# Optimization experiments

Hardware: AMD Instinct MI355X
Metric: run time of the kernel (lower is better)

Reference implementation:

```python
import jax, jax.numpy as jnp
import numpy as np

Z, N, K, W = 131072, 64, 64, 32


def setup_inputs() -> dict:
    key = jax.random.key(0)
    k1, k2, k3 = jax.random.split(key, 3)
    features = jax.random.normal(k1, (Z, N), dtype=jnp.float32)
    # dense realization of the CG-derived mixing tensor 'wkij'
    mixing_matrix = jax.random.normal(k2, (W, K, N, N), dtype=jnp.float32) * 0.05
    weight = jax.random.normal(k3, (W,), dtype=jnp.float32)
    return {"features": features, "mixing_matrix": mixing_matrix, "weight": weight}


def reference(features, mixing_matrix, weight):
    # torch: einsum('w,wkij,zi,zj->zk', weight, mixing_matrix, features, features)
    # Contract the small path axis w first -> [K, N, N] (cheap, tiny output),
    # then the bilinear square over z. einsum chooses a GEMM-style path; the
    # [Z, N, N] outer-product side is the memory-bound part.
    M = jnp.einsum('w,wkij->kij', weight, mixing_matrix)  # [K, N, N]
    out = jnp.einsum('kij,zi,zj->zk', M, features, features)  # [Z, K]
    return out
```

## Files before the change

### kernel.cpp

```cpp
#include <hip/hip_runtime.h>
#include <stdint.h>

typedef __attribute__((ext_vector_type(8))) short short8;
typedef __attribute__((ext_vector_type(4))) float f32x4;
typedef __attribute__((ext_vector_type(2))) float v2f;

#define NCHUNK 32
#define BROWS  136
#define XROWD  130

__device__ __forceinline__ unsigned short f2bf_rne(float f) {
  unsigned u = __builtin_bit_cast(unsigned, f);
  u += 0x7fffu + ((u >> 16) & 1u);
  return (unsigned short)(u >> 16);
}
__device__ __forceinline__ unsigned pack_bf2(float p0, float p1) {
  return __builtin_amdgcn_perm(__builtin_bit_cast(unsigned, p1),
                               __builtin_bit_cast(unsigned, p0), 0x07060302u);
}

__global__ __launch_bounds__(256) void prep_kernel(const float* __restrict__ mix,
                                                   const float* __restrict__ wgt,
                                                   unsigned short* __restrict__ Bp) {
  __shared__ float4 red[256];
  const int tid = threadIdx.x;
  const int ws  = tid >> 6;
  const int tt  = tid & 63;
  const int t4  = blockIdx.x * 64 + tt;
  const float4* m4 = (const float4*)mix;
  float ax = 0.f, ay = 0.f, az = 0.f, aw = 0.f;
#pragma unroll
  for (int wi = 0; wi < 8; ++wi) {
    const int w = ws * 8 + wi;
    const float s = wgt[w];
    const float4 v = m4[w * 65536 + t4];
    ax += s * v.x; ay += s * v.y; az += s * v.z; aw += s * v.w;
  }
  red[tid] = (float4){ax, ay, az, aw};
  __syncthreads();
  if (tid < 64) {
    const float4 a = red[tid], b = red[tid + 64], c = red[tid + 128], d = red[tid + 192];
    ushort4 r;
    r.x = f2bf_rne(a.x + b.x + c.x + d.x);
    r.y = f2bf_rne(a.y + b.y + c.y + d.y);
    r.z = f2bf_rne(a.z + b.z + c.z + d.z);
    r.w = f2bf_rne(a.w + b.w + c.w + d.w);
    ((ushort4*)Bp)[blockIdx.x * 64 + tid] = r;
  }
}

__global__ __launch_bounds__(256, 2) void gemm_kernel(const float* __restrict__ X,
                                                      const unsigned short* __restrict__ Bp,
                                                      float* __restrict__ out) {
  __shared__ unsigned short ldsB[2][64 * BROWS];
  __shared__ unsigned ldsX[64 * XROWD];

  const int tid  = threadIdx.x;
  const int lane = tid & 63;
  const int wv   = tid >> 6;
  const int m    = lane & 15;
  const int q    = lane >> 4;
  const int zblk = blockIdx.x * 256;

  {
    const float4* X4 = (const float4*)(X + (size_t)zblk * 64);
    const int rr = lane;
    const int ms = rr & 15;
    const int fd = (rr >> 4) & 1;
    const int ih = rr >> 5;
    const int zl = wv * 64 + fd * 32 + ms;
    const int zh = zl + 16;
    const int dcol = wv * 32 + ms * 2 + fd;
#pragma unroll
    for (int c4 = 0; c4 < 8; ++c4) {
      const float4 ve = X4[zl * 16 + ih * 8 + c4];
      const float4 vo = X4[zh * 16 + ih * 8 + c4];
      float ae[4], ao[4];
      *(float4*)ae = ve; *(float4*)ao = vo;
      const int i0 = ih * 32 + c4 * 4;
#pragma unroll
      for (int r = 0; r < 4; ++r) {
        const unsigned pk = (unsigned)f2bf_rne(ae[r]) | ((unsigned)f2bf_rne(ao[r]) << 16);
        ldsX[(i0 + r) * XROWD + dcol] = pk;
      }
    }
  }
  {
#pragma unroll
    for (int it = 0; it < 4; ++it) {
      const int lin = tid + it * 256;
      const int row = lin >> 4;
      const int cc  = lin & 15;
      const uint4 v = *(const uint4*)(Bp + row * 4096 + cc * 8);
      *(uint4*)(&ldsB[0][row * BROWS + cc * 8]) = v;
    }
  }

  v2f jv2[4][8];
  {
    const float4* X4g = (const float4*)X;
#pragma unroll
    for (int f = 0; f < 4; ++f) {
      const int zg = zblk + wv * 64 + f * 16 + m;
#pragma unroll
      for (int h = 0; h < 2; ++h) {
        const float4 a = X4g[zg * 16 + h * 8 + q * 2];
        const float4 b = X4g[zg * 16 + h * 8 + q * 2 + 1];
        jv2[f][h * 4 + 0] = v2f{a.x, a.y};
        jv2[f][h * 4 + 1] = v2f{a.z, a.w};
        jv2[f][h * 4 + 2] = v2f{b.x, b.y};
        jv2[f][h * 4 + 3] = v2f{b.z, b.w};
      }
    }
  }

  f32x4 acc[4][4];
#pragma unroll
  for (int f = 0; f < 4; ++f)
#pragma unroll
    for (int g = 0; g < 4; ++g) acc[f][g] = f32x4{0.f, 0.f, 0.f, 0.f};

  __syncthreads();

  for (int c = 0; c < NCHUNK; ++c) {
    uint4 pre[4];
    const int cn = (c + 1) & (NCHUNK - 1);
#pragma unroll
    for (int it = 0; it < 4; ++it) {
      const int lin = tid + it * 256;
      const int row = lin >> 4;
      const int cc  = lin & 15;
      pre[it] = *(const uint4*)(Bp + row * 4096 + cn * 128 + cc * 8);
    }

    const unsigned short* Bl = ldsB[c & 1];

#pragma unroll
    for (int il = 0; il < 2; ++il) {
      const int i = c * 2 + il;
      const uint2 sv = *(const uint2*)(ldsX + i * XROWD + wv * 32 + m * 2);
      float sf[4];
      sf[0] = __builtin_bit_cast(float, sv.x << 16);
      sf[1] = __builtin_bit_cast(float, sv.x & 0xffff0000u);
      sf[2] = __builtin_bit_cast(float, sv.y << 16);
      sf[3] = __builtin_bit_cast(float, sv.y & 0xffff0000u);
#pragma unroll
      for (int h = 0; h < 2; ++h) {
        const unsigned short* bb = Bl + m * BROWS + il * 64 + h * 32 + q * 8;
        const short8 b0 = *(const short8*)(bb);
        const short8 b1 = *(const short8*)(bb + 16 * BROWS);
        const short8 b2 = *(const short8*)(bb + 32 * BROWS);
        const short8 b3 = *(const short8*)(bb + 48 * BROWS);
#pragma unroll
        for (int f = 0; f < 4; ++f) {
          const v2f s2 = v2f{sf[f], sf[f]};
          union { unsigned u[4]; short8 v; } A;
#pragma unroll
          for (int e = 0; e < 4; ++e) {
            const v2f pr = s2 * jv2[f][h * 4 + e];
            A.u[e] = pack_bf2(pr[0], pr[1]);
          }
          acc[f][0] = __builtin_amdgcn_mfma_f32_16x16x32_bf16(A.v, b0, acc[f][0], 0, 0, 0);
          acc[f][1] = __builtin_amdgcn_mfma_f32_16x16x32_bf16(A.v, b1, acc[f][1], 0, 0, 0);
          acc[f][2] = __builtin_amdgcn_mfma_f32_16x16x32_bf16(A.v, b2, acc[f][2], 0, 0, 0);
          acc[f][3] = __builtin_amdgcn_mfma_f32_16x16x32_bf16(A.v, b3, acc[f][3], 0, 0, 0);
        }
      }
    }

    {
      unsigned short* dst = ldsB[(c + 1) & 1];
#pragma unroll
      for (int it = 0; it < 4; ++it) {
        const int lin = tid + it * 256;
        const int row = lin >> 4;
        const int cc  = lin & 15;
        *(uint4*)(&dst[row * BROWS + cc * 8]) = pre[it];
      }
    }
    __syncthreads();
  }

#pragma unroll
  for (int f = 0; f < 4; ++f) {
    const int zr = zblk + wv * 64 + f * 16 + q * 4;
#pragma unroll
    for (int g = 0; g < 4; ++g)
#pragma unroll
      for (int r = 0; r < 4; ++r)
        out[(size_t)(zr + r) * 64 + g * 16 + m] = acc[f][g][r];
  }
}

extern "C" void kernel_launch(void* const* d_in, const int* in_sizes, int n_in,
                              void* d_out, int out_size, void* d_ws, size_t ws_size,
                              hipStream_t stream) {
  const float* X   = (const float*)d_in[0];
  const float* mix = (const float*)d_in[1];
  const float* wgt = (const float*)d_in[2];
  float* out = (float*)d_out;
  unsigned short* Bp = (unsigned short*)d_ws;

  prep_kernel<<<1024, 256, 0, stream>>>(mix, wgt, Bp);
  gemm_kernel<<<512, 256, 0, stream>>>(X, Bp, out);
}
```

Baseline: 163.9 us.

## Fold M into upper-triangular form and skip half the bilinear MFMA work

Adds a kernel that symmetrizes each M_k by adding the transpose into the upper triangle and zeroing the lower triangle. The GEMM can then skip the j<i half-blocks for the second half of the i chunks, cutting MFMA and A-operand construction work. The GEMM block also shrinks to 128 rows with higher occupancy (launch bounds 4, 1024 blocks). It streams the per-chunk scale features through a small double-buffered LDS array instead of staging a full transposed X tile. The trade-offs are an extra kernel launch, a second bf16 rounding of the summed M entries, and the B operand still being streamed for the skipped blocks.

Result: slower. 249.4 us (+52.2%).

```diff
diff --git a/kernel.cpp b/kernel.cpp
--- a/kernel.cpp
+++ b/kernel.cpp
@@ -7,12 +7,14 @@
 
 #define NCHUNK 32
 #define BROWS  136
-#define XROWD  130
 
 __device__ __forceinline__ unsigned short f2bf_rne(float f) {
   unsigned u = __builtin_bit_cast(unsigned, f);
   u += 0x7fffu + ((u >> 16) & 1u);
   return (unsigned short)(u >> 16);
+}
+__device__ __forceinline__ float bf2f(unsigned short s) {
+  return __builtin_bit_cast(float, ((unsigned)s) << 16);
 }
 __device__ __forceinline__ unsigned pack_bf2(float p0, float p1) {
   return __builtin_amdgcn_perm(__builtin_bit_cast(unsigned, p1),
@@ -49,59 +51,54 @@
   }
 }
 
-__global__ __launch_bounds__(256, 2) void gemm_kernel(const float* __restrict__ X,
+__global__ __launch_bounds__(256) void symm_kernel(unsigned short* __restrict__ Bp) {
+  unsigned short* B = Bp + (size_t)blockIdx.x * 4096;
+  for (int t = threadIdx.x; t < 4096; t += 256) {
+    const int i = t >> 6, j = t & 63;
+    if (i < j) {
+      const int tt = (j << 6) | i;
+      const float a = bf2f(B[t]);
+      const float b = bf2f(B[tt]);
+      B[t]  = f2bf_rne(a + b);
+      B[tt] = 0;
+    }
+  }
+}
+
+__global__ __launch_bounds__(256, 4) void gemm_kernel(const float* __restrict__ X,
                                                       const unsigned short* __restrict__ Bp,
                                                       float* __restrict__ out) {
   __shared__ unsigned short ldsB[2][64 * BROWS];
-  __shared__ unsigned ldsX[64 * XROWD];
+  __shared__ unsigned short sH[2][2][128];
 
   const int tid  = threadIdx.x;
   const int lane = tid & 63;
   const int wv   = tid >> 6;
   const int m    = lane & 15;
   const int q    = lane >> 4;
-  const int zblk = blockIdx.x * 256;
-
-  {
-    const float4* X4 = (const float4*)(X + (size_t)zblk * 64);
-    const int rr = lane;
-    const int ms = rr & 15;
-    const int fd = (rr >> 4) & 1;
-    const int ih = rr >> 5;
-    const int zl = wv * 64 + fd * 32 + ms;
-    const int zh = zl + 16;
-    const int dcol = wv * 32 + ms * 2 + fd;
-#pragma unroll
-    for (int c4 = 0; c4 < 8; ++c4) {
-      const float4 ve = X4[zl * 16 + ih * 8 + c4];
-      const float4 vo = X4[zh * 16 + ih * 8 + c4];
-      float ae[4], ao[4];
-      *(float4*)ae = ve; *(float4*)ao = vo;
-      const int i0 = ih * 32 + c4 * 4;
-#pragma unroll
-      for (int r = 0; r < 4; ++r) {
-        const unsigned pk = (unsigned)f2bf_rne(ae[r]) | ((unsigned)f2bf_rne(ao[r]) << 16);
-        ldsX[(i0 + r) * XROWD + dcol] = pk;
-      }
-    }
-  }
-  {
-#pragma unroll
-    for (int it = 0; it < 4; ++it) {
-      const int lin = tid + it * 256;
-      const int row = lin >> 4;
-      const int cc  = lin & 15;
-      const uint4 v = *(const uint4*)(Bp + row * 4096 + cc * 8);
-      *(uint4*)(&ldsB[0][row * BROWS + cc * 8]) = v;
-    }
-  }
-
-  v2f jv2[4][8];
+  const int zblk = blockIdx.x * 128;
+
+#pragma unroll
+  for (int it = 0; it < 4; ++it) {
+    const int lin = tid + it * 256;
+    const int row = lin >> 4;
+    const int cc  = lin & 15;
+    *(uint4*)(&ldsB[0][row * BROWS + cc * 8]) = *(const uint4*)(Bp + row * 4096 + cc * 8);
+  }
+  if (tid < 128) {
+    const float2 xp = *(const float2*)(X + (size_t)(zblk + tid) * 64);
+    const int d  = (tid >> 5) * 16 + (tid & 15);
+    const int hf = (tid >> 4) & 1;
+    sH[0][0][d * 2 + hf] = f2bf_rne(xp.x);
+    sH[0][1][d * 2 + hf] = f2bf_rne(xp.y);
+  }
+
+  v2f jv2[2][8];
   {
     const float4* X4g = (const float4*)X;
 #pragma unroll
-    for (int f = 0; f < 4; ++f) {
-      const int zg = zblk + wv * 64 + f * 16 + m;
+    for (int f = 0; f < 2; ++f) {
+      const int zg = zblk + wv * 32 + f * 16 + m;
 #pragma unroll
       for (int h = 0; h < 2; ++h) {
         const float4 a = X4g[zg * 16 + h * 8 + q * 2];
@@ -114,17 +111,17 @@
     }
   }
 
-  f32x4 acc[4][4];
-#pragma unroll
-  for (int f = 0; f < 4; ++f)
+  f32x4 acc[2][4];
+#pragma unroll
+  for (int f = 0; f < 2; ++f)
 #pragma unroll
     for (int g = 0; g < 4; ++g) acc[f][g] = f32x4{0.f, 0.f, 0.f, 0.f};
 
   __syncthreads();
 
-  for (int c = 0; c < NCHUNK; ++c) {
+  auto chunk_body = [&](int c, bool full) {
+    const int cn = (c + 1) & (NCHUNK - 1);
     uint4 pre[4];
-    const int cn = (c + 1) & (NCHUNK - 1);
 #pragma unroll
     for (int it = 0; it < 4; ++it) {
       const int lin = tid + it * 256;
@@ -132,28 +129,26 @@
       const int cc  = lin & 15;
       pre[it] = *(const uint4*)(Bp + row * 4096 + cn * 128 + cc * 8);
     }
+    float2 spre = {0.f, 0.f};
+    if (tid < 128)
+      spre = *(const float2*)(X + (size_t)(zblk + tid) * 64 + cn * 2);
 
     const unsigned short* Bl = ldsB[c & 1];
-
 #pragma unroll
     for (int il = 0; il < 2; ++il) {
-      const int i = c * 2 + il;
-      const uint2 sv = *(const uint2*)(ldsX + i * XROWD + wv * 32 + m * 2);
-      float sf[4];
-      sf[0] = __builtin_bit_cast(float, sv.x << 16);
-      sf[1] = __builtin_bit_cast(float, sv.x & 0xffff0000u);
-      sf[2] = __builtin_bit_cast(float, sv.y << 16);
-      sf[3] = __builtin_bit_cast(float, sv.y & 0xffff0000u);
-#pragma unroll
-      for (int h = 0; h < 2; ++h) {
+      const unsigned sv = *(const unsigned*)(&sH[c & 1][il][(wv * 16 + m) * 2]);
+      const float s0 = __builtin_bit_cast(float, sv << 16);
+      const float s1 = __builtin_bit_cast(float, sv & 0xffff0000u);
+      auto hblk = [&](int h) {
         const unsigned short* bb = Bl + m * BROWS + il * 64 + h * 32 + q * 8;
         const short8 b0 = *(const short8*)(bb);
         const short8 b1 = *(const short8*)(bb + 16 * BROWS);
         const short8 b2 = *(const short8*)(bb + 32 * BROWS);
         const short8 b3 = *(const short8*)(bb + 48 * BROWS);
 #pragma unroll
-        for (int f = 0; f < 4; ++f) {
-          const v2f s2 = v2f{sf[f], sf[f]};
+        for (int f = 0; f < 2; ++f) {
+          const float sf_ = f ? s1 : s0;
+          const v2f s2 = v2f{sf_, sf_};
           union { unsigned u[4]; short8 v; } A;
 #pragma unroll
           for (int e = 0; e < 4; ++e) {
@@ -165,7 +160,9 @@
           acc[f][2] = __builtin_amdgcn_mfma_f32_16x16x32_bf16(A.v, b2, acc[f][2], 0, 0, 0);
           acc[f][3] = __builtin_amdgcn_mfma_f32_16x16x32_bf16(A.v, b3, acc[f][3], 0, 0, 0);
         }
-      }
+      };
+      if (full) hblk(0);
+      hblk(1);
     }
 
     {
@@ -177,13 +174,22 @@
         const int cc  = lin & 15;
         *(uint4*)(&dst[row * BROWS + cc * 8]) = pre[it];
       }
+      if (tid < 128) {
+        const int d  = (tid >> 5) * 16 + (tid & 15);
+        const int hf = (tid >> 4) & 1;
+        sH[(c + 1) & 1][0][d * 2 + hf] = f2bf_rne(spre.x);
+        sH[(c + 1) & 1][1][d * 2 + hf] = f2bf_rne(spre.y);
+      }
     }
     __syncthreads();
-  }
-
-#pragma unroll
-  for (int f = 0; f < 4; ++f) {
-    const int zr = zblk + wv * 64 + f * 16 + q * 4;
+  };
+
+  for (int c = 0; c < 16; ++c)      chunk_body(c, true);
+  for (int c = 16; c < NCHUNK; ++c) chunk_body(c, false);
+
+#pragma unroll
+  for (int f = 0; f < 2; ++f) {
+    const int zr = zblk + wv * 32 + f * 16 + q * 4;
 #pragma unroll
     for (int g = 0; g < 4; ++g)
 #pragma unroll
@@ -202,5 +208,6 @@
   unsigned short* Bp = (unsigned short*)d_ws;
 
   prep_kernel<<<1024, 256, 0, stream>>>(mix, wgt, Bp);
-  gemm_kernel<<<512, 256, 0, stream>>>(X, Bp, out);
-}
+  symm_kernel<<<64, 256, 0, stream>>>(Bp);
+  gemm_kernel<<<1024, 256, 0, stream>>>(X, Bp, out);
+}
```
